# Kernel optimization log

Hardware: AMD Instinct MI355X
Metric: run time of the kernel (lower is better)

Reference implementation:

```python
import jax, jax.numpy as jnp
import numpy as np

B, N, DIM = 16, 1024, 512
H, KD, D = 16, 32, 128          # num_heads, key_dim, d = attn_ratio*key_dim
DH = H * D                      # 2048
HQKV = DH + 2 * H * KD          # 3072
RES = 32
SCALE = KD ** -0.5
EPS = 1e-5


def _make_bias_idxs():
    ii = np.arange(N)
    px, py = ii // RES, ii % RES
    dx = np.abs(px[:, None] - px[None, :])
    dy = np.abs(py[:, None] - py[None, :])
    return (dx * RES + dy).astype(np.int32)  # (N, N), values in [0, RES*RES)


def setup_inputs() -> dict:
    key = jax.random.key(0)
    ks = jax.random.split(key, 6)
    return {
        "x": jax.random.normal(ks[0], (B, N, DIM), jnp.float32),
        "gamma": jnp.ones((DIM,), jnp.float32),
        "beta": jnp.zeros((DIM,), jnp.float32),
        "qkv_w": jax.random.normal(ks[1], (HQKV, DIM), jnp.float32) * 0.02,
        "qkv_b": jax.random.normal(ks[2], (HQKV,), jnp.float32) * 0.02,
        "proj_w": jax.random.normal(ks[3], (DIM, DH), jnp.float32) * 0.02,
        "proj_b": jax.random.normal(ks[4], (DIM,), jnp.float32) * 0.02,
        "attention_biases": jax.random.normal(ks[5], (H, RES * RES), jnp.float32) * 0.02,
        "bias_idxs": jnp.asarray(_make_bias_idxs()),
    }


def reference(x, gamma, beta, qkv_w, qkv_b, proj_w, proj_b, attention_biases, bias_idxs):
    # LayerNorm
    mu = jnp.mean(x, axis=-1, keepdims=True)
    var = jnp.mean(jnp.square(x - mu), axis=-1, keepdims=True)
    xn = (x - mu) * jax.lax.rsqrt(var + EPS) * gamma + beta
    # QKV projection -> (B, H, N, kd+kd+d)
    qkv = (xn @ qkv_w.T + qkv_b).reshape(B, N, H, 2 * KD + D).transpose(0, 2, 1, 3)
    q, k, v = qkv[..., :KD], qkv[..., KD:2 * KD], qkv[..., 2 * KD:]
    # Relative-position bias gather: (H, N, N)
    bias = attention_biases[:, bias_idxs]
    attn = jnp.einsum("bhnk,bhmk->bhnm", q, k) * SCALE + bias
    attn = jax.nn.softmax(attn, axis=-1)
    out = jnp.einsum("bhnm,bhmd->bhnd", attn, v)  # (B, H, N, D)
    out = out.transpose(0, 2, 1, 3).reshape(B, N, DH)
    return out @ proj_w.T + proj_b
```

## Files before the change

kernel.cpp:

```cpp
#include <hip/hip_runtime.h>

#define DIM_   512
#define NSEQ   1024
#define BB     16
#define HH     16
#define KD_    32
#define DD_    128
#define LDQKV  3072
#define DH_    2048
#define SCALE_ 0.17677669529663687f

typedef __bf16 bf16x8 __attribute__((ext_vector_type(8)));
typedef float  f32x4  __attribute__((ext_vector_type(4)));
typedef unsigned int u32x4v __attribute__((ext_vector_type(4)));

typedef __attribute__((address_space(1))) const unsigned int guint;
typedef __attribute__((address_space(3))) unsigned int luint;
#define GLL16(gp, lp) __builtin_amdgcn_global_load_lds((guint*)(gp), (luint*)(lp), 16, 0, 0)

static __device__ __forceinline__ unsigned short f2bf(float f) {
  unsigned int u = __builtin_bit_cast(unsigned int, f);
  u += 0x7fffu + ((u >> 16) & 1u);
  return (unsigned short)(u >> 16);
}

__global__ __launch_bounds__(256) void cvt_kernel(const float* __restrict__ in,
                                                  unsigned short* __restrict__ out,
                                                  int n) {
  int i = blockIdx.x * 256 + threadIdx.x;
  if (i < n) out[i] = f2bf(in[i]);
}

__global__ __launch_bounds__(256) void ln_kernel(const float* __restrict__ x,
                                                 const float* __restrict__ gamma,
                                                 const float* __restrict__ beta,
                                                 unsigned short* __restrict__ xn) {
  int row = blockIdx.x, t = threadIdx.x;
  const float* xr = x + (size_t)row * DIM_;
  float2 v = *(const float2*)(xr + t * 2);
  float s = v.x + v.y, sq = v.x * v.x + v.y * v.y;
#pragma unroll
  for (int off = 32; off; off >>= 1) {
    s  += __shfl_xor(s, off, 64);
    sq += __shfl_xor(sq, off, 64);
  }
  __shared__ float red[8];
  int wid = t >> 6, lane = t & 63;
  if (lane == 0) { red[wid * 2] = s; red[wid * 2 + 1] = sq; }
  __syncthreads();
  float S  = red[0] + red[2] + red[4] + red[6];
  float SQ = red[1] + red[3] + red[5] + red[7];
  float mu   = S * (1.f / DIM_);
  float var  = SQ * (1.f / DIM_) - mu * mu;
  float rstd = rsqrtf(var + 1e-5f);
  int c = t * 2;
  xn[(size_t)row * DIM_ + c]     = f2bf((v.x - mu) * rstd * gamma[c]     + beta[c]);
  xn[(size_t)row * DIM_ + c + 1] = f2bf((v.y - mu) * rstd * gamma[c + 1] + beta[c + 1]);
}

template <typename OUT, bool VREMAP, bool VSPLIT>
__global__ __launch_bounds__(256) void gemm_gll(const unsigned short* __restrict__ A, int lda,
                                                const unsigned short* __restrict__ W, int ldb,
                                                const float* __restrict__ bias,
                                                OUT* __restrict__ C, int ldc,
                                                int K,
                                                unsigned short* __restrict__ vTout) {
  __shared__ unsigned short a_sm[128][64];
  __shared__ unsigned short b_sm[128][64];
  int tid = threadIdx.x;
  int lane = tid & 63, w = tid >> 6;
  int quad = lane >> 4, l15 = lane & 15;
  int wr = w >> 1, wc = w & 1;
  long tm = (long)blockIdx.y * 128, tn = (long)blockIdx.x * 128;
  int srow = w * 8 + (lane >> 3), scol = (lane & 7) * 8;

  f32x4 acc[4][4] = {};

  for (int k0 = 0; k0 < K; k0 += 64) {
    __syncthreads();
#pragma unroll
    for (int it = 0; it < 4; it++) {
      if constexpr (VREMAP) {
        int kk = k0 + scol;
        GLL16(A + (size_t)(tm + it * 32 + srow) * LDQKV + (kk >> 7) * 192 + 64 + (kk & 127),
              &a_sm[it * 32 + w * 8][0]);
      } else {
        GLL16(A + (tm + it * 32 + srow) * lda + k0 + scol, &a_sm[it * 32 + w * 8][0]);
      }
      GLL16(W + (tn + it * 32 + srow) * ldb + k0 + scol, &b_sm[it * 32 + w * 8][0]);
    }
    __syncthreads();
#pragma unroll
    for (int kk = 0; kk < 64; kk += 32) {
      bf16x8 af[4], bfr[4];
#pragma unroll
      for (int i = 0; i < 4; i++)
        af[i] = *(const bf16x8*)&a_sm[wr * 64 + i * 16 + l15][kk + quad * 8];
#pragma unroll
      for (int j = 0; j < 4; j++)
        bfr[j] = *(const bf16x8*)&b_sm[wc * 64 + j * 16 + l15][kk + quad * 8];
#pragma unroll
      for (int i = 0; i < 4; i++)
#pragma unroll
        for (int j = 0; j < 4; j++)
          acc[i][j] = __builtin_amdgcn_mfma_f32_16x16x32_bf16(af[i], bfr[j], acc[i][j], 0, 0, 0);
    }
  }
#pragma unroll
  for (int j = 0; j < 4; j++) {
    long col = tn + wc * 64 + j * 16 + l15;
    float bv = bias[col];
    bool vcol = false;
    size_t vtbase = 0;
    if constexpr (VSPLIT) {
      int cm = (int)(col % 192);
      vcol = cm >= 64;
      int h = (int)(col / 192), d = cm - 64;
      vtbase = ((size_t)h * 128 + d) * 1024;
    }
#pragma unroll
    for (int i = 0; i < 4; i++) {
      long row0 = tm + wr * 64 + i * 16 + quad * 4;
      if (VSPLIT && vcol) {
        int b = (int)(row0 >> 10), n = (int)(row0 & 1023);
        unsigned long long pkv =
            (unsigned long long)f2bf(acc[i][j][0] + bv) |
            ((unsigned long long)f2bf(acc[i][j][1] + bv) << 16) |
            ((unsigned long long)f2bf(acc[i][j][2] + bv) << 32) |
            ((unsigned long long)f2bf(acc[i][j][3] + bv) << 48);
        *(unsigned long long*)(vTout + (size_t)b * 16 * 131072 + vtbase + n) = pkv;
      } else {
#pragma unroll
        for (int r = 0; r < 4; r++) {
          float val = acc[i][j][r] + bv;
          if constexpr (__is_same(OUT, float))
            C[(row0 + r) * ldc + col] = val;
          else
            C[(row0 + r) * ldc + col] = f2bf(val);
        }
      }
    }
  }
}

__global__ __launch_bounds__(256) void attn_kernel(const unsigned short* __restrict__ qkv,
                                                   const unsigned short* __restrict__ vT,
                                                   const float* __restrict__ ab,
                                                   unsigned short* attn_out) {
  __shared__ float lut[1024];
  __shared__ unsigned short v_sm[2][128][64];
  __shared__ unsigned short k_sm[2][64][32];

  int tid = threadIdx.x;
  int lane = tid & 63, w = tid >> 6;
  int quad = lane >> 4, l15 = lane & 15;

  int id = blockIdx.x;
  int bh = ((id >> 7) << 3) | (id & 7);
  int qb = (id >> 3) & 15;
  int b = bh >> 4, h = bh & 15;
  const unsigned short* base = qkv + (size_t)b * NSEQ * LDQKV + h * 192;
  const unsigned short* vTh = vT + (size_t)bh * 131072;

  for (int t = tid; t < 1024; t += 256) lut[t] = ab[h * 1024 + t];

  int qg = qb * 64 + w * 16 + l15;
  bf16x8 qf = *(const bf16x8*)(base + (size_t)qg * LDQKV + quad * 8);

  int rx = qg >> 5, ry = qg & 31;
  int dy_pre[8];
#pragma unroll
  for (int i = 0; i < 8; i++) {
    int cy = ((i >> 2) << 4) | (quad * 4 + (i & 3));
    int d = ry - cy; dy_pre[i] = d < 0 ? -d : d;
  }

  int ixA = ((quad & 1) * 32 + l15) * 4;
  int ixB = ixA + 64;
  bool hiq = quad >= 2;

  f32x4 accO[8] = {};
  float l_r = 0.f;

  int vrow   = lane >> 3;
  int vchunk = (lane & 7) ^ (lane >> 3);
  int krow   = w * 16 + (lane >> 2);
  int kcol   = (lane & 3) * 8;

#pragma unroll
  for (int i = 0; i < 4; i++) {
    int r0 = (w * 4 + i) * 8;
    GLL16(vTh + (size_t)(r0 + vrow) * 1024 + vchunk * 8, &v_sm[0][r0][0]);
  }
  GLL16(base + (size_t)krow * LDQKV + 32 + kcol, &k_sm[0][w * 16][0]);

  for (int kt = 0; kt < 16; kt++) {
    int cur = kt & 1;
    __syncthreads();
    if (kt < 15) {
      int nxt = cur ^ 1;
#pragma unroll
      for (int i = 0; i < 4; i++) {
        int r0 = (w * 4 + i) * 8;
        GLL16(vTh + (size_t)(r0 + vrow) * 1024 + (kt + 1) * 64 + vchunk * 8, &v_sm[nxt][r0][0]);
      }
      GLL16(base + (size_t)((kt + 1) * 64 + krow) * LDQKV + 32 + kcol, &k_sm[nxt][w * 16][0]);
    }

    f32x4 st[4];
#pragma unroll
    for (int nb = 0; nb < 4; nb++) {
      bf16x8 kf = *(const bf16x8*)&k_sm[cur][nb * 16 + l15][quad * 8];
      f32x4 z = {};
      st[nb] = __builtin_amdgcn_mfma_f32_16x16x32_bf16(kf, qf, z, 0, 0, 0);
    }

    int d0 = rx - 2 * kt;     int dxa = d0 < 0 ? -d0 : d0;
    int d1 = d0 - 1;          int dxb = d1 < 0 ? -d1 : d1;
    int lb0 = dxa << 5, lb1 = dxb << 5;

    unsigned pk[8];
#pragma unroll
    for (int nb = 0; nb < 4; nb++) {
      int lb = (nb & 2) ? lb1 : lb0;
#pragma unroll
      for (int t = 0; t < 2; t++) {
        float p0 = __expf(fmaf(st[nb][2 * t],     SCALE_, lut[lb + dy_pre[(nb & 1) * 4 + 2 * t]]));
        float p1 = __expf(fmaf(st[nb][2 * t + 1], SCALE_, lut[lb + dy_pre[(nb & 1) * 4 + 2 * t + 1]]));
        l_r += p0 + p1;
        unsigned short u0 = __builtin_bit_cast(unsigned short, (__bf16)p0);
        unsigned short u1 = __builtin_bit_cast(unsigned short, (__bf16)p1);
        pk[nb * 2 + t] = (unsigned)u0 | ((unsigned)u1 << 16);
      }
    }

#pragma unroll
    for (int kc = 0; kc < 2; kc++) {
      int s0 = (int)pk[4 * kc + 0], s1 = (int)pk[4 * kc + 1];
      int s2 = (int)pk[4 * kc + 2], s3 = (int)pk[4 * kc + 3];
      unsigned a0 = (unsigned)__builtin_amdgcn_ds_bpermute(ixA, s0);
      unsigned a1 = (unsigned)__builtin_amdgcn_ds_bpermute(ixA, s1);
      unsigned a2 = (unsigned)__builtin_amdgcn_ds_bpermute(ixA, s2);
      unsigned a3 = (unsigned)__builtin_amdgcn_ds_bpermute(ixA, s3);
      unsigned b0 = (unsigned)__builtin_amdgcn_ds_bpermute(ixB, s0);
      unsigned b1 = (unsigned)__builtin_amdgcn_ds_bpermute(ixB, s1);
      unsigned b2 = (unsigned)__builtin_amdgcn_ds_bpermute(ixB, s2);
      unsigned b3 = (unsigned)__builtin_amdgcn_ds_bpermute(ixB, s3);
      u32x4v paw;
      paw.x = hiq ? a2 : a0;
      paw.y = hiq ? a3 : a1;
      paw.z = hiq ? b2 : b0;
      paw.w = hiq ? b3 : b1;
      bf16x8 paf = __builtin_bit_cast(bf16x8, paw);

#pragma unroll
      for (int db = 0; db < 8; db++) {
        bf16x8 vf = *(const bf16x8*)&v_sm[cur][db * 16 + l15][((kc * 4 + quad) ^ (l15 & 7)) * 8];
        accO[db] = __builtin_amdgcn_mfma_f32_16x16x32_bf16(paf, vf, accO[db], 0, 0, 0);
      }
    }
  }

  l_r += __shfl_xor(l_r, 16, 64);
  l_r += __shfl_xor(l_r, 32, 64);

#pragma unroll
  for (int r = 0; r < 4; r++) {
    float lr = __shfl(l_r, quad * 4 + r, 16);
    float inv = 1.f / lr;
    int row = qb * 64 + w * 16 + quad * 4 + r;
    size_t obase = ((size_t)b * NSEQ + row) * LDQKV + h * 192 + 64;
#pragma unroll
    for (int db = 0; db < 8; db++)
      attn_out[obase + db * 16 + l15] = f2bf(accO[db][r] * inv);
  }
}

extern "C" void kernel_launch(void* const* d_in, const int* in_sizes, int n_in,
                              void* d_out, int out_size, void* d_ws, size_t ws_size,
                              hipStream_t stream) {
  const float* x      = (const float*)d_in[0];
  const float* gamma  = (const float*)d_in[1];
  const float* beta   = (const float*)d_in[2];
  const float* qkv_w  = (const float*)d_in[3];
  const float* qkv_b  = (const float*)d_in[4];
  const float* proj_w = (const float*)d_in[5];
  const float* proj_b = (const float*)d_in[6];
  const float* ab     = (const float*)d_in[7];

  char* ws = (char*)d_ws;
  unsigned short* xn    = (unsigned short*)(ws);
  unsigned short* wqkv  = (unsigned short*)(ws + (size_t)16 * 1048576);
  unsigned short* wproj = (unsigned short*)(ws + (size_t)19 * 1048576);
  unsigned short* qkv   = (unsigned short*)(ws + (size_t)21 * 1048576);
  unsigned short* vT    = (unsigned short*)(ws + (size_t)117 * 1048576);
  float* out = (float*)d_out;

  cvt_kernel<<<dim3(6144), dim3(256), 0, stream>>>(qkv_w, wqkv, 3072 * 512);
  cvt_kernel<<<dim3(4096), dim3(256), 0, stream>>>(proj_w, wproj, 512 * 2048);
  ln_kernel<<<dim3(16384), dim3(256), 0, stream>>>(x, gamma, beta, xn);
  gemm_gll<unsigned short, false, true><<<dim3(24, 128), dim3(256), 0, stream>>>(
      xn, 512, wqkv, 512, qkv_b, qkv, 3072, 512, vT);
  attn_kernel<<<dim3(4096), dim3(256), 0, stream>>>(qkv, vT, ab, qkv);
  gemm_gll<float, true, false><<<dim3(4, 128), dim3(256), 0, stream>>>(
      qkv, 3072, wproj, 2048, proj_b, out, 512, 2048, (unsigned short*)nullptr);
}
```

Baseline: 468.4 us.

## Stage attention K/V tiles through registers and compute row sums via MFMA

Replaces the double-buffered global_load_lds prefetch with register prefetch into a single LDS buffer, adding a second barrier per tile. The softmax exp becomes exp2 with the log2(e) factor folded into the bias table and the scale. The row-sum accumulation moves from scalar adds plus shuffles to an extra MFMA against a ones vector, which also sums the bf16-rounded probabilities. The intent is to cut LDS footprint, raising occupancy, and to trim VALU work in the inner loop, at the cost of extra register pressure and synchronisation.

After: 623.6 us. +33.1%, slower.

```diff
diff --git a/kernel.cpp b/kernel.cpp
--- a/kernel.cpp
+++ b/kernel.cpp
@@ -9,6 +9,7 @@
 #define LDQKV  3072
 #define DH_    2048
 #define SCALE_ 0.17677669529663687f
+#define SCALE2_ 0.2550353739f
 
 typedef __bf16 bf16x8 __attribute__((ext_vector_type(8)));
 typedef float  f32x4  __attribute__((ext_vector_type(4)));
@@ -148,8 +149,8 @@
                                                    const float* __restrict__ ab,
                                                    unsigned short* attn_out) {
   __shared__ float lut[1024];
-  __shared__ unsigned short v_sm[2][128][64];
-  __shared__ unsigned short k_sm[2][64][32];
+  __shared__ unsigned short v_sm[128][64];
+  __shared__ unsigned short k_sm[64][32];
 
   int tid = threadIdx.x;
   int lane = tid & 63, w = tid >> 6;
@@ -162,7 +163,7 @@
   const unsigned short* base = qkv + (size_t)b * NSEQ * LDQKV + h * 192;
   const unsigned short* vTh = vT + (size_t)bh * 131072;
 
-  for (int t = tid; t < 1024; t += 256) lut[t] = ab[h * 1024 + t];
+  for (int t = tid; t < 1024; t += 256) lut[t] = ab[h * 1024 + t] * 1.44269504f;
 
   int qg = qb * 64 + w * 16 + l15;
   bf16x8 qf = *(const bf16x8*)(base + (size_t)qg * LDQKV + quad * 8);
@@ -179,38 +180,46 @@
   int ixB = ixA + 64;
   bool hiq = quad >= 2;
 
+  u32x4v ow; ow.x = ow.y = ow.z = ow.w = 0x3F803F80u;
+  const bf16x8 onesf = __builtin_bit_cast(bf16x8, ow);
+
   f32x4 accO[8] = {};
-  float l_r = 0.f;
+  f32x4 accL = {};
 
   int vrow   = lane >> 3;
   int vchunk = (lane & 7) ^ (lane >> 3);
   int krow   = w * 16 + (lane >> 2);
   int kcol   = (lane & 3) * 8;
 
+  uint4 vreg[4]; uint4 kreg;
 #pragma unroll
   for (int i = 0; i < 4; i++) {
     int r0 = (w * 4 + i) * 8;
-    GLL16(vTh + (size_t)(r0 + vrow) * 1024 + vchunk * 8, &v_sm[0][r0][0]);
-  }
-  GLL16(base + (size_t)krow * LDQKV + 32 + kcol, &k_sm[0][w * 16][0]);
+    vreg[i] = *(const uint4*)(vTh + (size_t)(r0 + vrow) * 1024 + vchunk * 8);
+  }
+  kreg = *(const uint4*)(base + (size_t)krow * LDQKV + 32 + kcol);
 
   for (int kt = 0; kt < 16; kt++) {
-    int cur = kt & 1;
     __syncthreads();
+#pragma unroll
+    for (int i = 0; i < 4; i++)
+      *(uint4*)&v_sm[(w * 4 + i) * 8 + vrow][(lane & 7) * 8] = vreg[i];
+    *(uint4*)&k_sm[krow][kcol] = kreg;
+    __syncthreads();
+
     if (kt < 15) {
-      int nxt = cur ^ 1;
 #pragma unroll
       for (int i = 0; i < 4; i++) {
         int r0 = (w * 4 + i) * 8;
-        GLL16(vTh + (size_t)(r0 + vrow) * 1024 + (kt + 1) * 64 + vchunk * 8, &v_sm[nxt][r0][0]);
-      }
-      GLL16(base + (size_t)((kt + 1) * 64 + krow) * LDQKV + 32 + kcol, &k_sm[nxt][w * 16][0]);
+        vreg[i] = *(const uint4*)(vTh + (size_t)(r0 + vrow) * 1024 + (kt + 1) * 64 + vchunk * 8);
+      }
+      kreg = *(const uint4*)(base + (size_t)((kt + 1) * 64 + krow) * LDQKV + 32 + kcol);
     }
 
     f32x4 st[4];
 #pragma unroll
     for (int nb = 0; nb < 4; nb++) {
-      bf16x8 kf = *(const bf16x8*)&k_sm[cur][nb * 16 + l15][quad * 8];
+      bf16x8 kf = *(const bf16x8*)&k_sm[nb * 16 + l15][quad * 8];
       f32x4 z = {};
       st[nb] = __builtin_amdgcn_mfma_f32_16x16x32_bf16(kf, qf, z, 0, 0, 0);
     }
@@ -225,9 +234,8 @@
       int lb = (nb & 2) ? lb1 : lb0;
 #pragma unroll
       for (int t = 0; t < 2; t++) {
-        float p0 = __expf(fmaf(st[nb][2 * t],     SCALE_, lut[lb + dy_pre[(nb & 1) * 4 + 2 * t]]));
-        float p1 = __expf(fmaf(st[nb][2 * t + 1], SCALE_, lut[lb + dy_pre[(nb & 1) * 4 + 2 * t + 1]]));
-        l_r += p0 + p1;
+        float p0 = exp2f(fmaf(st[nb][2 * t],     SCALE2_, lut[lb + dy_pre[(nb & 1) * 4 + 2 * t]]));
+        float p1 = exp2f(fmaf(st[nb][2 * t + 1], SCALE2_, lut[lb + dy_pre[(nb & 1) * 4 + 2 * t + 1]]));
         unsigned short u0 = __builtin_bit_cast(unsigned short, (__bf16)p0);
         unsigned short u1 = __builtin_bit_cast(unsigned short, (__bf16)p1);
         pk[nb * 2 + t] = (unsigned)u0 | ((unsigned)u1 << 16);
@@ -255,19 +263,16 @@
 
 #pragma unroll
       for (int db = 0; db < 8; db++) {
-        bf16x8 vf = *(const bf16x8*)&v_sm[cur][db * 16 + l15][((kc * 4 + quad) ^ (l15 & 7)) * 8];
+        bf16x8 vf = *(const bf16x8*)&v_sm[db * 16 + l15][((kc * 4 + quad) ^ (l15 & 7)) * 8];
         accO[db] = __builtin_amdgcn_mfma_f32_16x16x32_bf16(paf, vf, accO[db], 0, 0, 0);
       }
-    }
-  }
-
-  l_r += __shfl_xor(l_r, 16, 64);
-  l_r += __shfl_xor(l_r, 32, 64);
+      accL = __builtin_amdgcn_mfma_f32_16x16x32_bf16(paf, onesf, accL, 0, 0, 0);
+    }
+  }
 
 #pragma unroll
   for (int r = 0; r < 4; r++) {
-    float lr = __shfl(l_r, quad * 4 + r, 16);
-    float inv = 1.f / lr;
+    float inv = 1.f / accL[r];
     int row = qb * 64 + w * 16 + quad * 4 + r;
     size_t obase = ((size_t)b * NSEQ + row) * LDQKV + h * 192 + 64;
 #pragma unroll
```
